# Kernel tuning notes

Measured on AMD Instinct MI355X. Metric: run time of the kernel, lower is better.

Reference implementation:

```python
import jax, jax.numpy as jnp
import numpy as np

NUM_CLASSES = 7
CLASS_WEIGHT = 1.0
BOX_WEIGHT = 1.0


def _linear_sum_assignment(cost):
    """Exact Hungarian via shortest augmenting paths (Jonker-Volgenant style).
    Matches scipy.optimize.linear_sum_assignment for rectangular matrices:
    returns (row_ind, col_ind) of length min(n, m), row_ind sorted ascending."""
    C = np.asarray(cost, dtype=np.float64)
    transposed = C.shape[0] > C.shape[1]
    if transposed:
        C = C.T
    n, m = C.shape  # n <= m
    u = np.zeros(n + 1)
    v = np.zeros(m + 1)
    p = np.zeros(m + 1, dtype=np.int64)    # p[j]: row matched to col j (1-based); 0 = free
    way = np.zeros(m + 1, dtype=np.int64)
    for i in range(1, n + 1):
        p[0] = i
        j0 = 0
        minv = np.full(m + 1, np.inf)
        used = np.zeros(m + 1, dtype=bool)
        while True:
            used[j0] = True
            i0 = p[j0]
            cur = C[i0 - 1] - u[i0] - v[1:]
            free = ~used[1:]
            better = free & (cur < minv[1:])
            minv[1:][better] = cur[better]
            way[1:][better] = j0
            masked = np.where(free, minv[1:], np.inf)
            j0n = int(np.argmin(masked)) + 1
            delta = masked[j0n - 1]
            uj = np.nonzero(used)[0]
            u[p[uj]] += delta
            v[uj] -= delta
            minv[1:][free] -= delta
            j0 = j0n
            if p[j0] == 0:
                break
        while j0 != 0:   # augment along alternating path
            j1 = way[j0]
            p[j0] = p[j1]
            j0 = j1
    cols = np.nonzero(p[1:] > 0)[0]
    rows = p[1:][cols] - 1
    if transposed:
        rows, cols = cols, rows
    order = np.argsort(rows)
    return rows[order], cols[order]


def _cost_matrices(pred_logits, pred_boxes, gt_labels, gt_boxes):
    """Batched cost: class_weight * (-log_softmax gathered at gt labels) + box_weight * L1 cdist on xyz."""
    B, Q, _ = pred_logits.shape
    M = gt_labels.shape[1]
    log_probs = jax.nn.log_softmax(pred_logits, axis=-1)                       # (B,Q,C)
    idx = jnp.broadcast_to(gt_labels[:, None, :], (B, Q, M))
    class_cost = -jnp.take_along_axis(log_probs, idx, axis=2)                  # (B,Q,M)
    box_cost = jnp.sum(jnp.abs(pred_boxes[:, :, None, :3] - gt_boxes[:, None, :, :3]), axis=-1)  # (B,Q,M)
    return CLASS_WEIGHT * class_cost + BOX_WEIGHT * box_cost


def _matched_loss(pred_logits, pred_boxes, gt_labels, gt_boxes, rows, cols):
    B = pred_logits.shape[0]
    bidx = jnp.arange(B)[:, None]
    ml = pred_logits[bidx, rows]          # (B,M,C) matched logits
    mb = pred_boxes[bidx, rows]           # (B,M,7) matched boxes
    gl = gt_labels[bidx, cols]            # (B,M)
    gb = gt_boxes[bidx, cols]             # (B,M,7)
    logp = jax.nn.log_softmax(ml, axis=-1)
    ce = -jnp.mean(jnp.take_along_axis(logp, gl[..., None], axis=-1)[..., 0], axis=1)  # (B,)
    l1 = jnp.mean(jnp.abs(mb - gb), axis=(1, 2))                                       # (B,)
    return jnp.mean(CLASS_WEIGHT * ce + BOX_WEIGHT * l1)


def setup_inputs() -> dict:
    key = jax.random.key(0)
    k1, k2, k3, k4 = jax.random.split(key, 4)
    B, Q, M = 128, 900, 100
    return {
        'pred_logits': jax.random.normal(k1, (B, Q, NUM_CLASSES), dtype=jnp.float32),
        'pred_boxes': jax.random.normal(k2, (B, Q, 7), dtype=jnp.float32),
        'gt_labels': jax.random.randint(k3, (B, M), 0, NUM_CLASSES, dtype=jnp.int32),
        'gt_boxes': jax.random.normal(k4, (B, M, 7), dtype=jnp.float32),
    }


def reference(pred_logits, pred_boxes, gt_labels, gt_boxes):
    B = pred_logits.shape[0]
    M = gt_labels.shape[1]
    # Assignment is done on detached costs (host-side), matching the original module.
    cost = np.asarray(_cost_matrices(pred_logits, pred_boxes, gt_labels, gt_boxes))
    rows = np.zeros((B, M), dtype=np.int64)
    cols = np.zeros((B, M), dtype=np.int64)
    for b in range(B):
        r, c = _linear_sum_assignment(cost[b])
        rows[b], cols[b] = r, c
    return _matched_loss(pred_logits, pred_boxes, gt_labels, gt_boxes,
                         jnp.asarray(rows), jnp.asarray(cols))
```

## Files before the change

kernel.cpp:

```cpp
#include <hip/hip_runtime.h>
#include <math.h>


#define NQ   900
#define NG   100
#define NC   7
#define CPL  15
#define ROUNDS 12
#define INFF __builtin_inff()

__device__ __forceinline__ float readlane_f(float x, int l) {
  return __int_as_float(__builtin_amdgcn_readlane(__float_as_int(x), l));
}
template<int CTRL>
__device__ __forceinline__ float dpp_min_step(float x) {
  int y = __builtin_amdgcn_update_dpp(__float_as_int(x), __float_as_int(x),
                                      CTRL, 0xf, 0xf, false);
  return fminf(x, __int_as_float(y));
}
__device__ __forceinline__ float wave_min_b(float x) {
  x = dpp_min_step<0x111>(x);
  x = dpp_min_step<0x112>(x);
  x = dpp_min_step<0x114>(x);
  x = dpp_min_step<0x118>(x);
  x = dpp_min_step<0x142>(x);
  x = dpp_min_step<0x143>(x);
  return __int_as_float(__builtin_amdgcn_readlane(__float_as_int(x), 63));
}
template<int CTRL>
__device__ __forceinline__ float dpp_add_step(float x) {
  int y = __builtin_amdgcn_update_dpp(0, __float_as_int(x),
                                      CTRL, 0xf, 0xf, true);
  return x + __int_as_float(y);
}
__device__ __forceinline__ float wave_sum_b(float x) {
  x = dpp_add_step<0x111>(x);
  x = dpp_add_step<0x112>(x);
  x = dpp_add_step<0x114>(x);
  x = dpp_add_step<0x118>(x);
  x = dpp_add_step<0x142>(x);
  x = dpp_add_step<0x143>(x);
  return __int_as_float(__builtin_amdgcn_readlane(__float_as_int(x), 63));
}
__device__ __forceinline__ void gl_lds16(const float* g, float* lds_base) {
  __builtin_amdgcn_global_load_lds(
      (const __attribute__((address_space(1))) unsigned int*)g,
      (__attribute__((address_space(3))) unsigned int*)lds_base, 16, 0, 0);
}
__device__ __forceinline__ float sel7v(float a0,float a1,float a2,float a3,
                                       float a4,float a5,float a6,int lab){
  float r = a0;
  r = lab==1 ? a1 : r;  r = lab==2 ? a2 : r;  r = lab==3 ? a3 : r;
  r = lab==4 ? a4 : r;  r = lab==5 ? a5 : r;  r = lab==6 ? a6 : r;
  return r;
}

__global__ __launch_bounds__(256, 1) void hungarian_fused_kernel(
    const float* __restrict__ logits, const float* __restrict__ pboxes,
    const int* __restrict__ glabels, const float* __restrict__ gboxes,
    float* __restrict__ out, float inv_B)
{
  const int b = blockIdx.x, tid = threadIdx.x;
  const int lane = tid & 63, w = tid >> 6;

  __shared__ __align__(16) float s_raw[NQ * NC];
  __shared__ __align__(16) float s_nlpT[NC * 1024];
  __shared__ __align__(16) float s_pb[960 * NC];
  __shared__ __align__(16) float s_gb[NG * NC];
  __shared__ __align__(16) int   s_glab[NG];
  __shared__ float s_u[NG + 1];
  __shared__ float s_v[CPL * 64];
  __shared__ int   s_p[NQ];
  __shared__ unsigned s_bid[NQ];
  __shared__ int   s_rmatch[NG];
  __shared__ float s_bm1[NG], s_bm2[NG];
  __shared__ int   s_bc[NG];
  __shared__ int   s_freelist[NG];
  __shared__ int   s_nfree;
  __shared__ float s_f1v[NG]; __shared__ int s_f1c[NG];
  __shared__ float s_f2v[NG]; __shared__ int s_f2c[NG];
  __shared__ int   s_mlist[128];

  {
    const float* Lg = logits + (size_t)b * NQ * NC;
    const float* Pg = pboxes + (size_t)b * NQ * NC;
    const float* Gg = gboxes + (size_t)b * NG * NC;
    const int*   Bg = glabels + (size_t)b * NG;
    #pragma unroll
    for (int t = 0; t < 7; t++) {
      int i = (t << 8) + tid;
      if (i < (NQ * NC) / 4) {
        gl_lds16(Lg + i * 4, s_raw + ((t << 8) + (w << 6)) * 4);
        gl_lds16(Pg + i * 4, s_pb  + ((t << 8) + (w << 6)) * 4);
      }
    }
    if (tid < (NG * NC) / 4) gl_lds16(Gg + tid * 4, s_gb + (w << 6) * 4);
    if (tid < NG / 4) gl_lds16((const float*)Bg + tid * 4, (float*)s_glab);
    for (int i = tid; i < (960 - NQ) * NC; i += 256) s_pb[NQ * NC + i] = 0.f;
    for (int c = tid; c < NQ; c += 256) { s_p[c] = 0x7fffffff; s_bid[c] = 0xFFFFFFFFu; }
    for (int i = tid; i < CPL * 64; i += 256) s_v[i] = 0.f;
    if (tid == 0) s_u[0] = 0.f;
  }
  __syncthreads();

  for (int i = tid; i < 960; i += 256) {
    int L = i & 63, t = i >> 6;
    int q = L * CPL + t;
    float o[NC];
    if (q < NQ) {
      float x[NC];
      #pragma unroll
      for (int c = 0; c < NC; c++) x[c] = s_raw[q * NC + c];
      float mx = x[0];
      #pragma unroll
      for (int c = 1; c < NC; c++) mx = fmaxf(mx, x[c]);
      float tt[NC]; float se = 0.f;
      #pragma unroll
      for (int c = 0; c < NC; c++) { tt[c] = x[c] - mx; se += __expf(tt[c]); }
      float lg = __logf(se);
      #pragma unroll
      for (int c = 0; c < NC; c++) o[c] = lg - tt[c];
    } else {
      #pragma unroll
      for (int c = 0; c < NC; c++) o[c] = INFF;
    }
    #pragma unroll
    for (int c = 0; c < NC; c++) s_nlpT[c * 1024 + t * 64 + L] = o[c];
  }
  __syncthreads();

  const bool lval = (lane < NQ / CPL);
  float cpx[CPL], cpy[CPL], cpz[CPL];
  #pragma unroll
  for (int t = 0; t < CPL; t++) {
    int c = lane * CPL + t;
    cpx[t]=s_pb[c*NC+0]; cpy[t]=s_pb[c*NC+1]; cpz[t]=s_pb[c*NC+2];
  }

  for (int rl = 0; rl < 25; rl++) {
    int r = w * 25 + rl;
    int lab = s_glab[r];
    float gx = s_gb[r*NC+0], gy = s_gb[r*NC+1], gz = s_gb[r*NC+2];
    float m1 = INFF; int c1t = 0;
    #pragma unroll
    for (int t = 0; t < CPL; t++) {
      float nl = s_nlpT[lab*1024 + t*64 + lane];
      float bs = fabsf(cpx[t]-gx)+fabsf(cpy[t]-gy)+fabsf(cpz[t]-gz);
      float cost = nl + bs;
      bool lt1 = cost < m1;
      c1t = lt1 ? t : c1t;
      m1 = fminf(m1, cost);
    }
    float w1 = wave_min_b(m1);
    unsigned long long mk = __ballot(m1 == w1);
    int src = (int)__builtin_ctzll(mk);
    int col = __builtin_amdgcn_readlane(lane * CPL + c1t, src);
    if (lane == 0) {
      s_u[r + 1] = w1;
      s_bc[r] = col;
      atomicMin(&s_p[col], r + 1);
    }
  }
  __syncthreads();
  for (int c = tid; c < NQ; c += 256) if (s_p[c] == 0x7fffffff) s_p[c] = 0;
  if (tid < NG) {
    int c = s_bc[tid];
    s_rmatch[tid] = (s_p[c] == tid + 1) ? c + 1 : 0;
  }
  __syncthreads();

  for (int round = 0; round < ROUNDS; round++) {
    if (tid == 0) s_nfree = 0;
    __syncthreads();
    if (tid < NG && s_rmatch[tid] == 0) {
      int ix = atomicAdd(&s_nfree, 1);
      s_freelist[ix] = tid;
    }
    __syncthreads();
    int nf = s_nfree;
    if (nf == 0) break;
    for (int fi = w; fi < nf; fi += 4) {
      int r = s_freelist[fi];
      int lab = s_glab[r];
      float gx = s_gb[r*NC+0], gy = s_gb[r*NC+1], gz = s_gb[r*NC+2];
      float m1 = INFF, m2 = INFF; int c1t = 0;
      #pragma unroll
      for (int t = 0; t < CPL; t++) {
        float nl = s_nlpT[lab*1024 + t*64 + lane];
        float vv = s_v[t*64 + lane];
        float bs = fabsf(cpx[t]-gx)+fabsf(cpy[t]-gy)+fabsf(cpz[t]-gz);
        float cost = (nl + bs) - vv;
        bool lt1 = cost < m1;
        m2 = lt1 ? m1 : fminf(m2, cost);
        c1t = lt1 ? t : c1t;
        m1 = fminf(m1, cost);
      }
      float w1 = wave_min_b(m1);
      unsigned long long mk = __ballot(m1 == w1);
      int src = (int)__builtin_ctzll(mk);
      int col1 = __builtin_amdgcn_readlane(lane * CPL + c1t, src);
      float alt = (lane == src) ? m2 : m1;
      float w2 = wave_min_b(alt);
      if (lane == 0) {
        s_bm1[r] = w1; s_bm2[r] = w2; s_bc[r] = col1;
        atomicMin(&s_bid[col1],
                  (__float_as_uint(w1) & 0xFFFFFF80u) | (unsigned)(r + 1));
      }
    }
    __syncthreads();
    for (int fi = tid; fi < nf; fi += 256) {
      int r = s_freelist[fi];
      int c = s_bc[r];
      if ((s_bid[c] & 0x7Fu) == (unsigned)(r + 1)) {
        int dold = s_p[c];
        s_p[c] = r + 1;
        s_rmatch[r] = c + 1;
        if (dold > 0) s_rmatch[dold - 1] = 0;
        s_u[r + 1] = s_bm2[r];
        s_v[(c % CPL) * 64 + (c / CPL)] -= (s_bm2[r] - s_bm1[r]);
      }
    }
    __syncthreads();
    for (int fi = tid; fi < nf; fi += 256)
      s_bid[s_bc[s_freelist[fi]]] = 0xFFFFFFFFu;
    __syncthreads();
  }

  if (tid == 0) s_nfree = 0;
  __syncthreads();
  if (tid < NG && s_rmatch[tid] == 0) {
    int ix = atomicAdd(&s_nfree, 1);
    s_freelist[ix] = tid;
  }
  __syncthreads();
  const int nfinal = s_nfree;
  if (nfinal > 0) {
    for (int fi = w; fi < nfinal; fi += 4) {
      int r = s_freelist[fi];
      int lab = s_glab[r];
      float gx = s_gb[r*NC+0], gy = s_gb[r*NC+1], gz = s_gb[r*NC+2];
      float m1 = INFF;
      #pragma unroll
      for (int t = 0; t < CPL; t++) {
        float nl = s_nlpT[lab*1024 + t*64 + lane];
        float vv = s_v[t*64 + lane];
        float bs = fabsf(cpx[t]-gx)+fabsf(cpy[t]-gy)+fabsf(cpz[t]-gz);
        m1 = fminf(m1, (nl + bs) - vv);
      }
      float w1 = wave_min_b(m1);
      if (lane == 0) s_u[r + 1] = w1;
    }
    __syncthreads();
  }

  if (nfinal > 0) {
  unsigned fmask = 0;
  if (lval) {
    #pragma unroll
    for (int t = 0; t < CPL; t++)
      if (s_p[lane * CPL + t] == 0) fmask |= (1u << t);
  }

  auto top2row = [&](int lab, float gx, float gy, float gz,
                     float &o1v, int &o1c, float &o2v, int &o2c) {
    float m1 = INFF, m2 = INFF; int c1 = 0, c2 = 0;
    #pragma unroll
    for (int t = 0; t < CPL; t++) {
      float nl = s_nlpT[lab*1024 + t*64 + lane];
      float bs = fabsf(cpx[t]-gx)+fabsf(cpy[t]-gy)+fabsf(cpz[t]-gz);
      float cost = nl + bs;
      cost = ((fmask >> t) & 1u) ? cost : INFF;
      bool lt1 = cost < m1;
      bool lt2 = cost < m2;
      c2 = lt1 ? c1 : (lt2 ? t : c2);
      m2 = lt1 ? m1 : fminf(m2, cost);
      c1 = lt1 ? t : c1;
      m1 = fminf(m1, cost);
    }
    float w1 = wave_min_b(m1);
    unsigned long long mk = __ballot(m1 == w1);
    int src = (int)__builtin_ctzll(mk);
    int col1 = __builtin_amdgcn_readlane(lane * CPL + c1, src);
    float alt = (lane == src) ? m2 : m1;
    int  altc = (lane == src) ? c2 : c1;
    float w2 = wave_min_b(alt);
    unsigned long long mk2 = __ballot(alt == w2);
    int src2 = (int)__builtin_ctzll(mk2);
    int col2 = __builtin_amdgcn_readlane(lane * CPL + altc, src2);
    o1v = w1; o1c = col1; o2v = w2; o2c = col2;
  };

  for (int rl = 0; rl < 25; rl++) {
    int r = w * 25 + rl;
    int lab = s_glab[r];
    float gx = s_gb[r*NC+0], gy = s_gb[r*NC+1], gz = s_gb[r*NC+2];
    float v1, v2; int cc1, cc2;
    top2row(lab, gx, gy, gz, v1, cc1, v2, cc2);
    if (lane == 0) {
      s_f1v[r] = v1; s_f1c[r] = cc1; s_f2v[r] = v2; s_f2c[r] = cc2;
    }
  }
  __syncthreads();
  if (w != 0) return;

  volatile float* vu = s_u;

  const bool r1ok = (lane < NG - 64);
  int   rlab0 = s_glab[lane];
  float rgx0 = s_gb[lane*NC+0], rgy0 = s_gb[lane*NC+1], rgz0 = s_gb[lane*NC+2];
  int   rlab1 = 0; float rgx1=0.f, rgy1=0.f, rgz1=0.f;
  if (r1ok) {
    int r = 64 + lane;
    rlab1 = s_glab[r];
    rgx1 = s_gb[r*NC+0]; rgy1 = s_gb[r*NC+1]; rgz1 = s_gb[r*NC+2];
  }
  float ru0 = vu[lane + 1];
  float ru1 = r1ok ? vu[lane + 65] : 0.f;
  float rf1v0 = s_f1v[lane];       int rf1c0 = s_f1c[lane];
  float rf2v0 = s_f2v[lane];       int rf2c0 = s_f2c[lane];
  float rf1v1 = r1ok ? s_f1v[64+lane] : INFF; int rf1c1 = r1ok ? s_f1c[64+lane] : -1;
  float rf2v1 = r1ok ? s_f2v[64+lane] : INFF; int rf2c1 = r1ok ? s_f2c[64+lane] : -1;

  bool lose0 = (s_rmatch[lane] == 0);
  bool lose1 = r1ok && (s_rmatch[64 + lane] == 0);
  unsigned long long fm0 = __ballot(lose0);
  unsigned long long fm1 = __ballot(lose1);

  int NM = 0;
  #pragma unroll
  for (int t = 0; t < CPL; t++) {
    int c = lane * CPL + t;
    bool has = lval && (s_p[c] > 0);
    unsigned long long m = __ballot(has);
    int pos = NM + (int)__popcll(m & ((1ull << lane) - 1ull));
    if (has) s_mlist[pos] = c;
    NM += (int)__popcll(m);
  }

  int   mcol[2]  = {-1,-1};
  int   mprow[2] = {0,0};
  float mpu[2]   = {0.f,0.f};
  float mv[2]    = {0.f,0.f};
  float mx[2]={0,0}, my[2]={0,0}, mz[2]={0,0};
  float mn0[2],mn1[2],mn2[2],mn3[2],mn4[2],mn5[2],mn6[2];
  #pragma unroll
  for (int k = 0; k < 2; k++) { mn0[k]=0;mn1[k]=0;mn2[k]=0;mn3[k]=0;mn4[k]=0;mn5[k]=0;mn6[k]=0; }
  #pragma unroll
  for (int k = 0; k < 2; k++) {
    int s = lane + (k << 6);
    if (s < NM) {
      int c = s_mlist[s];
      int cq = c / CPL, ct = c - cq * CPL;
      mcol[k] = c;
      mx[k] = s_pb[c*NC+0]; my[k] = s_pb[c*NC+1]; mz[k] = s_pb[c*NC+2];
      mn0[k] = s_nlpT[0*1024 + ct*64 + cq];
      mn1[k] = s_nlpT[1*1024 + ct*64 + cq];
      mn2[k] = s_nlpT[2*1024 + ct*64 + cq];
      mn3[k] = s_nlpT[3*1024 + ct*64 + cq];
      mn4[k] = s_nlpT[4*1024 + ct*64 + cq];
      mn5[k] = s_nlpT[5*1024 + ct*64 + cq];
      mn6[k] = s_nlpT[6*1024 + ct*64 + cq];
      mprow[k] = s_p[c];
      mpu[k] = vu[mprow[k]];
      mv[k] = s_v[ct * 64 + cq];
    }
  }

  float dsl[2]; int wsl[2];

  for (int half = 0; half < 2; half++) {
    unsigned long long fm = half ? fm1 : fm0;
    while (fm) {
      int bit = (int)__builtin_ctzll(fm);
      fm &= fm - 1;
      int rfree = bit + (half ? 65 : 1);
      dsl[0] = INFF; dsl[1] = INFF; wsl[0] = 0; wsl[1] = 0;
      unsigned usedm = 0;
      float bfv = INFF; int bfc = -1, bfprev = 0;
      int i0 = rfree;
      int ro0 = rfree - 1;
      float u_i0 = readlane_f((ro0 >> 6) ? ru1 : ru0, ro0 & 63);
      int j0p = 0;
      float minVal = 0.f;
      int jf = -1, jfprev = 0;

      for (int it = 0; it < 128; it++) {
        int ro = i0 - 1, rown = ro & 63, rs = ro >> 6;
        int   lab = __builtin_amdgcn_readlane(rs ? rlab1 : rlab0, rown);
        float gx = readlane_f(rs ? rgx1 : rgx0, rown);
        float gy = readlane_f(rs ? rgy1 : rgy0, rown);
        float gz = readlane_f(rs ? rgz1 : rgz0, rown);
        float hs = minVal - u_i0;
        float f1v = readlane_f(rs ? rf1v1 : rf1v0, rown);
        int   f1c = __builtin_amdgcn_readlane(rs ? rf1c1 : rf1c0, rown);
        float cbf = f1v + hs;
        if (cbf < bfv) { bfv = cbf; bfc = f1c; bfprev = j0p; }
        float lb = INFF; int bk = 0;
        #pragma unroll
        for (int k = 0; k < 2; k++) {
          bool gate = ((lane + (k << 6)) < NM) && !((usedm >> k) & 1u);
          float nl = sel7v(mn0[k],mn1[k],mn2[k],mn3[k],mn4[k],mn5[k],mn6[k],lab);
          float bs = fabsf(mx[k]-gx)+fabsf(my[k]-gy)+fabsf(mz[k]-gz);
          float rr = ((nl + bs) + hs) - mv[k];
          bool imp = gate && (rr < dsl[k]);
          dsl[k] = imp ? rr : dsl[k];
          wsl[k] = imp ? j0p : wsl[k];
          float cand = gate ? dsl[k] : INFF;
          bool bt = cand < lb;
          bk = bt ? k : bk;
          lb = fminf(lb, cand);
        }
        float dm = wave_min_b(lb);
        if (bfv <= dm) { minVal = bfv; jf = bfc; jfprev = bfprev; break; }
        unsigned long long msk = __ballot(lb == dm);
        int src = (int)__builtin_ctzll(msk);
        int spk = __builtin_amdgcn_readlane((bk << 6) | lane, src);
        minVal = dm;
        int so = spk & 63, sk = spk >> 6;
        usedm |= (lane == so) ? (1u << sk) : 0u;
        i0  = __builtin_amdgcn_readlane(sk ? mprow[1] : mprow[0], so);
        u_i0 = readlane_f(sk ? mpu[1] : mpu[0], so);
        j0p = spk + 1;
      }
      if (jf < 0) { jf = bfc; jfprev = bfprev; minVal = bfv; }

      if (lane == 0) vu[rfree] += minVal;
      #pragma unroll
      for (int k = 0; k < 2; k++) {
        if ((usedm >> k) & 1u) {
          float a = minVal - dsl[k];
          mv[k] -= a;
          vu[mprow[k]] += a;
        }
      }
      __threadfence_block();

      int pred = jfprev;
      int nr;
      if (pred == 0) nr = rfree;
      else {
        int s = pred - 1;
        nr = __builtin_amdgcn_readlane((s >> 6) ? mprow[1] : mprow[0], s & 63);
      }
      if (lane == 0) s_p[jf] = nr;
      {
        int cq = jf / CPL, ct = jf - cq * CPL;
        float nx = s_pb[jf*NC+0], ny = s_pb[jf*NC+1], nz = s_pb[jf*NC+2];
        float a0 = s_nlpT[0*1024 + ct*64 + cq];
        float a1 = s_nlpT[1*1024 + ct*64 + cq];
        float a2 = s_nlpT[2*1024 + ct*64 + cq];
        float a3 = s_nlpT[3*1024 + ct*64 + cq];
        float a4 = s_nlpT[4*1024 + ct*64 + cq];
        float a5 = s_nlpT[5*1024 + ct*64 + cq];
        float a6 = s_nlpT[6*1024 + ct*64 + cq];
        int kk = NM >> 6;
        if (lane == (NM & 63) && NM < 128) {
          if (kk == 0) {
            mcol[0]=jf; mx[0]=nx; my[0]=ny; mz[0]=nz; mprow[0]=nr; mv[0]=0.f;
            mn0[0]=a0;mn1[0]=a1;mn2[0]=a2;mn3[0]=a3;mn4[0]=a4;mn5[0]=a5;mn6[0]=a6;
          } else {
            mcol[1]=jf; mx[1]=nx; my[1]=ny; mz[1]=nz; mprow[1]=nr; mv[1]=0.f;
            mn0[1]=a0;mn1[1]=a1;mn2[1]=a2;mn3[1]=a3;mn4[1]=a4;mn5[1]=a5;mn6[1]=a6;
          }
        }
        NM++;
      }
      while (pred) {
        int s = pred - 1, so = s & 63, sk = s >> 6;
        int np = __builtin_amdgcn_readlane(sk ? wsl[1] : wsl[0], so);
        int nr2;
        if (np == 0) nr2 = rfree;
        else {
          int s2 = np - 1;
          nr2 = __builtin_amdgcn_readlane((s2 >> 6) ? mprow[1] : mprow[0], s2 & 63);
        }
        int sc = __builtin_amdgcn_readlane(sk ? mcol[1] : mcol[0], so);
        if (lane == so) { if (sk) mprow[1] = nr2; else mprow[0] = nr2; }
        if (lane == 0) s_p[sc] = nr2;
        pred = np;
      }
      __threadfence_block();

      ru0 = vu[lane + 1];
      if (r1ok) ru1 = vu[lane + 65];
      #pragma unroll
      for (int k = 0; k < 2; k++)
        if ((lane + (k << 6)) < NM) mpu[k] = vu[mprow[k]];

      if (lane == (jf / CPL)) fmask &= ~(1u << (jf - (jf / CPL) * CPL));
      if (rf1c0 == jf) { rf1v0 = rf2v0; rf1c0 = rf2c0; rf2c0 = -1; rf2v0 = INFF; }
      else if (rf2c0 == jf) { rf2c0 = -1; rf2v0 = INFF; }
      if (rf1c1 == jf) { rf1v1 = rf2v1; rf1c1 = rf2c1; rf2c1 = -1; rf2v1 = INFF; }
      else if (rf2c1 == jf) { rf2c1 = -1; rf2v1 = INFF; }
      unsigned long long need0 = __ballot(rf1c0 < 0);
      unsigned long long need1 = __ballot(r1ok && (rf1c1 < 0));
      while (need0) {
        int rb = (int)__builtin_ctzll(need0); need0 &= need0 - 1;
        int lab = __builtin_amdgcn_readlane(rlab0, rb);
        float gx = readlane_f(rgx0, rb), gy = readlane_f(rgy0, rb), gz = readlane_f(rgz0, rb);
        float v1, v2; int cc1, cc2;
        top2row(lab, gx, gy, gz, v1, cc1, v2, cc2);
        if (lane == rb) { rf1v0=v1; rf1c0=cc1; rf2v0=v2; rf2c0=cc2; }
      }
      while (need1) {
        int rb = (int)__builtin_ctzll(need1); need1 &= need1 - 1;
        int lab = __builtin_amdgcn_readlane(rlab1, rb);
        float gx = readlane_f(rgx1, rb), gy = readlane_f(rgy1, rb), gz = readlane_f(rgz1, rb);
        float v1, v2; int cc1, cc2;
        top2row(lab, gx, gy, gz, v1, cc1, v2, cc2);
        if (lane == rb) { rf1v1=v1; rf1c1=cc1; rf2v1=v2; rf2c1=cc2; }
      }
    }
  }
  }

  if (w != 0) return;
  {
    float ce = 0.f, l1 = 0.f;
    if (lval) {
      #pragma unroll
      for (int t = 0; t < CPL; t++) {
        int c = lane * CPL + t;
        int pr = s_p[c];
        if (pr > 0) {
          int g = pr - 1;
          int lg = s_glab[g];
          ce += s_nlpT[lg*1024 + t*64 + lane];
          float s = 0.f;
          #pragma unroll
          for (int d7 = 0; d7 < 7; d7++) s += fabsf(s_pb[c*NC+d7] - s_gb[g*NC+d7]);
          l1 += s;
        }
      }
    }
    float tot = ce * (1.f / NG) + l1 * (1.f / (NG * 7.f));
    tot = wave_sum_b(tot);
    if (lane == 0) atomicAdd(out, tot * inv_B);
  }
}

extern "C" void kernel_launch(void* const* d_in, const int* in_sizes, int n_in,
                              void* d_out, int out_size, void* d_ws, size_t ws_size,
                              hipStream_t stream) {
  const float* logits  = (const float*)d_in[0];
  const float* pboxes  = (const float*)d_in[1];
  const int*   glabels = (const int*)d_in[2];
  const float* gboxes  = (const float*)d_in[3];
  float* out = (float*)d_out;
  const int B = in_sizes[0] / (NQ * NC);

  hipMemsetAsync(out, 0, sizeof(float), stream);
  hungarian_fused_kernel<<<dim3(B), dim3(256), 0, stream>>>(
      logits, pboxes, glabels, gboxes, out, 1.0f / (float)B);
}
```

Measured before the change: 131.1 us.

## Replace atomic free-list with ballot bitmasks, fuse top-2 reduction, cache v in registers

The auction rounds now build the free-row set with wave ballots into two 64-bit masks instead of an atomic-append free list. This removes a barrier and the atomic contention, and one barrier per round is dropped by folding the s_bid reset into the next round. The two sequential wave-min reductions for best and second-best are merged into one DPP top-2 reduction. Column prices are cached in registers per round, and ROUNDS drops from 12 to 10. Fewer rounds push more unmatched rows onto the slower fallback path, and dropping the trailing barrier relies on the next round's ballot barrier for ordering.

```diff
diff --git a/kernel.cpp b/kernel.cpp
--- a/kernel.cpp
+++ b/kernel.cpp
@@ -6,7 +6,7 @@
 #define NG   100
 #define NC   7
 #define CPL  15
-#define ROUNDS 12
+#define ROUNDS 10
 #define INFF __builtin_inff()
 
 __device__ __forceinline__ float readlane_f(float x, int l) {
@@ -26,6 +26,29 @@
   x = dpp_min_step<0x142>(x);
   x = dpp_min_step<0x143>(x);
   return __int_as_float(__builtin_amdgcn_readlane(__float_as_int(x), 63));
+}
+template<int CTRL>
+__device__ __forceinline__ void dpp_min2_step(float &a, float &b) {
+  const int INFI = 0x7f800000;
+  float a2 = __int_as_float(__builtin_amdgcn_update_dpp(
+      INFI, __float_as_int(a), CTRL, 0xf, 0xf, false));
+  float b2 = __int_as_float(__builtin_amdgcn_update_dpp(
+      INFI, __float_as_int(b), CTRL, 0xf, 0xf, false));
+  float lo = fminf(a, a2);
+  float hi = fmaxf(a, a2);
+  b = fminf(hi, fminf(b, b2));
+  a = lo;
+}
+__device__ __forceinline__ void wave_min2_b(float m1, float m2,
+                                            float &o1, float &o2) {
+  dpp_min2_step<0x111>(m1, m2);
+  dpp_min2_step<0x112>(m1, m2);
+  dpp_min2_step<0x114>(m1, m2);
+  dpp_min2_step<0x118>(m1, m2);
+  dpp_min2_step<0x142>(m1, m2);
+  dpp_min2_step<0x143>(m1, m2);
+  o1 = readlane_f(m1, 63);
+  o2 = readlane_f(m2, 63);
 }
 template<int CTRL>
 __device__ __forceinline__ float dpp_add_step(float x) {
@@ -75,8 +98,7 @@
   __shared__ int   s_rmatch[NG];
   __shared__ float s_bm1[NG], s_bm2[NG];
   __shared__ int   s_bc[NG];
-  __shared__ int   s_freelist[NG];
-  __shared__ int   s_nfree;
+  __shared__ unsigned long long s_fm[2];
   __shared__ float s_f1v[NG]; __shared__ int s_f1c[NG];
   __shared__ float s_f2v[NG]; __shared__ int s_f2c[NG];
   __shared__ int   s_mlist[128];
@@ -170,82 +192,106 @@
   __syncthreads();
 
   for (int round = 0; round < ROUNDS; round++) {
-    if (tid == 0) s_nfree = 0;
+    if (w == 0) {
+      unsigned long long m = __ballot(s_rmatch[lane] == 0);
+      if (lane == 0) s_fm[0] = m;
+    } else if (w == 1) {
+      unsigned long long m = __ballot((lane < NG - 64) && s_rmatch[64 + lane] == 0);
+      if (lane == 0) s_fm[1] = m;
+    }
     __syncthreads();
-    if (tid < NG && s_rmatch[tid] == 0) {
-      int ix = atomicAdd(&s_nfree, 1);
-      s_freelist[ix] = tid;
+    const unsigned long long fm0r = s_fm[0], fm1r = s_fm[1];
+    if ((fm0r | fm1r) == 0) break;
+    float vreg[CPL];
+    #pragma unroll
+    for (int t = 0; t < CPL; t++) vreg[t] = s_v[t*64 + lane];
+    {
+      unsigned long long mm0 = fm0r, mm1 = fm1r;
+      int idx = 0;
+      while (mm0 | mm1) {
+        int r;
+        if (mm0) { int b2 = (int)__builtin_ctzll(mm0); mm0 &= mm0 - 1; r = b2; }
+        else     { int b2 = (int)__builtin_ctzll(mm1); mm1 &= mm1 - 1; r = 64 + b2; }
+        if ((idx++ & 3) != w) continue;
+        int lab = s_glab[r];
+        float gx = s_gb[r*NC+0], gy = s_gb[r*NC+1], gz = s_gb[r*NC+2];
+        float m1 = INFF, m2 = INFF; int c1t = 0;
+        #pragma unroll
+        for (int t = 0; t < CPL; t++) {
+          float nl = s_nlpT[lab*1024 + t*64 + lane];
+          float bs = fabsf(cpx[t]-gx)+fabsf(cpy[t]-gy)+fabsf(cpz[t]-gz);
+          float cost = (nl + bs) - vreg[t];
+          bool lt1 = cost < m1;
+          m2 = lt1 ? m1 : fminf(m2, cost);
+          c1t = lt1 ? t : c1t;
+          m1 = fminf(m1, cost);
+        }
+        float w1, w2;
+        wave_min2_b(m1, m2, w1, w2);
+        unsigned long long mk = __ballot(m1 == w1);
+        int src = (int)__builtin_ctzll(mk);
+        int col1 = __builtin_amdgcn_readlane(lane * CPL + c1t, src);
+        if (lane == 0) {
+          s_bm1[r] = w1; s_bm2[r] = w2; s_bc[r] = col1;
+          atomicMin(&s_bid[col1],
+                    (__float_as_uint(w1) & 0xFFFFFF80u) | (unsigned)(r + 1));
+        }
+      }
     }
     __syncthreads();
-    int nf = s_nfree;
-    if (nf == 0) break;
-    for (int fi = w; fi < nf; fi += 4) {
-      int r = s_freelist[fi];
-      int lab = s_glab[r];
-      float gx = s_gb[r*NC+0], gy = s_gb[r*NC+1], gz = s_gb[r*NC+2];
-      float m1 = INFF, m2 = INFF; int c1t = 0;
-      #pragma unroll
-      for (int t = 0; t < CPL; t++) {
-        float nl = s_nlpT[lab*1024 + t*64 + lane];
-        float vv = s_v[t*64 + lane];
-        float bs = fabsf(cpx[t]-gx)+fabsf(cpy[t]-gy)+fabsf(cpz[t]-gz);
-        float cost = (nl + bs) - vv;
-        bool lt1 = cost < m1;
-        m2 = lt1 ? m1 : fminf(m2, cost);
-        c1t = lt1 ? t : c1t;
-        m1 = fminf(m1, cost);
-      }
-      float w1 = wave_min_b(m1);
-      unsigned long long mk = __ballot(m1 == w1);
-      int src = (int)__builtin_ctzll(mk);
-      int col1 = __builtin_amdgcn_readlane(lane * CPL + c1t, src);
-      float alt = (lane == src) ? m2 : m1;
-      float w2 = wave_min_b(alt);
-      if (lane == 0) {
-        s_bm1[r] = w1; s_bm2[r] = w2; s_bc[r] = col1;
-        atomicMin(&s_bid[col1],
-                  (__float_as_uint(w1) & 0xFFFFFF80u) | (unsigned)(r + 1));
+    if (tid < NG) {
+      bool wasfree = (tid < 64) ? ((fm0r >> tid) & 1ull)
+                                : ((fm1r >> (tid - 64)) & 1ull);
+      if (wasfree) {
+        int c = s_bc[tid];
+        if ((s_bid[c] & 0x7Fu) == (unsigned)(tid + 1)) {
+          int dold = s_p[c];
+          s_p[c] = tid + 1;
+          s_rmatch[tid] = c + 1;
+          if (dold > 0) s_rmatch[dold - 1] = 0;
+          s_u[tid + 1] = s_bm2[tid];
+          s_v[(c % CPL) * 64 + (c / CPL)] -= (s_bm2[tid] - s_bm1[tid]);
+        }
       }
     }
     __syncthreads();
-    for (int fi = tid; fi < nf; fi += 256) {
-      int r = s_freelist[fi];
-      int c = s_bc[r];
-      if ((s_bid[c] & 0x7Fu) == (unsigned)(r + 1)) {
-        int dold = s_p[c];
-        s_p[c] = r + 1;
-        s_rmatch[r] = c + 1;
-        if (dold > 0) s_rmatch[dold - 1] = 0;
-        s_u[r + 1] = s_bm2[r];
-        s_v[(c % CPL) * 64 + (c / CPL)] -= (s_bm2[r] - s_bm1[r]);
-      }
-    }
-    __syncthreads();
-    for (int fi = tid; fi < nf; fi += 256)
-      s_bid[s_bc[s_freelist[fi]]] = 0xFFFFFFFFu;
-    __syncthreads();
-  }
-
-  if (tid == 0) s_nfree = 0;
-  __syncthreads();
-  if (tid < NG && s_rmatch[tid] == 0) {
-    int ix = atomicAdd(&s_nfree, 1);
-    s_freelist[ix] = tid;
-  }
-  __syncthreads();
-  const int nfinal = s_nfree;
+    if (tid < NG) {
+      bool wasfree = (tid < 64) ? ((fm0r >> tid) & 1ull)
+                                : ((fm1r >> (tid - 64)) & 1ull);
+      if (wasfree) s_bid[s_bc[tid]] = 0xFFFFFFFFu;
+    }
+  }
+  __syncthreads();
+
+  if (w == 0) {
+    unsigned long long m = __ballot(s_rmatch[lane] == 0);
+    if (lane == 0) s_fm[0] = m;
+  } else if (w == 1) {
+    unsigned long long m = __ballot((lane < NG - 64) && s_rmatch[64 + lane] == 0);
+    if (lane == 0) s_fm[1] = m;
+  }
+  __syncthreads();
+  const unsigned long long ff0 = s_fm[0], ff1 = s_fm[1];
+  const int nfinal = __popcll(ff0) + __popcll(ff1);
   if (nfinal > 0) {
-    for (int fi = w; fi < nfinal; fi += 4) {
-      int r = s_freelist[fi];
+    float vreg[CPL];
+    #pragma unroll
+    for (int t = 0; t < CPL; t++) vreg[t] = s_v[t*64 + lane];
+    unsigned long long mm0 = ff0, mm1 = ff1;
+    int idx = 0;
+    while (mm0 | mm1) {
+      int r;
+      if (mm0) { int b2 = (int)__builtin_ctzll(mm0); mm0 &= mm0 - 1; r = b2; }
+      else     { int b2 = (int)__builtin_ctzll(mm1); mm1 &= mm1 - 1; r = 64 + b2; }
+      if ((idx++ & 3) != w) continue;
       int lab = s_glab[r];
       float gx = s_gb[r*NC+0], gy = s_gb[r*NC+1], gz = s_gb[r*NC+2];
       float m1 = INFF;
       #pragma unroll
       for (int t = 0; t < CPL; t++) {
         float nl = s_nlpT[lab*1024 + t*64 + lane];
-        float vv = s_v[t*64 + lane];
         float bs = fabsf(cpx[t]-gx)+fabsf(cpy[t]-gy)+fabsf(cpz[t]-gz);
-        m1 = fminf(m1, (nl + bs) - vv);
+        m1 = fminf(m1, (nl + bs) - vreg[t]);
       }
       float w1 = wave_min_b(m1);
       if (lane == 0) s_u[r + 1] = w1;
@@ -321,10 +367,8 @@
   float rf1v1 = r1ok ? s_f1v[64+lane] : INFF; int rf1c1 = r1ok ? s_f1c[64+lane] : -1;
   float rf2v1 = r1ok ? s_f2v[64+lane] : INFF; int rf2c1 = r1ok ? s_f2c[64+lane] : -1;
 
-  bool lose0 = (s_rmatch[lane] == 0);
-  bool lose1 = r1ok && (s_rmatch[64 + lane] == 0);
-  unsigned long long fm0 = __ballot(lose0);
-  unsigned long long fm1 = __ballot(lose1);
+  unsigned long long fm0 = ff0;
+  unsigned long long fm1 = ff1;
 
   int NM = 0;
   #pragma unroll
```

After: 130.4 us. Within noise of the previous version (-0.5%).
